# Performance work log

Hardware: AMD Instinct MI355X
Metric: run time of the kernel (lower is better)

## Reference

```python
import jax, jax.numpy as jnp
import numpy as np

T_MAX = 20  # max_seq_length


def setup_inputs() -> dict:
    key = jax.random.key(0)
    ks = jax.random.split(key, 24)
    B, H, A, V, Tc = 64, 512, 512, 50257, 19
    s = 0.02
    inp = {}
    inp["features"] = jax.random.normal(ks[0], (B, H), jnp.float32)
    inp["captions"] = jax.random.randint(ks[1], (B, Tc), 0, V)
    lens = jax.random.randint(ks[2], (B, 1), 1, T_MAX + 1)
    inp["lengths"] = -jnp.sort(-lens, axis=0)  # descending so sort_ind is identity
    inp["embed_table"] = jax.random.uniform(ks[3], (V, H), jnp.float32, -0.1, 0.1)
    # LSTM cell (PyTorch layout): input = [emb; attended] -> 2H
    inp["W_ih"] = jax.random.normal(ks[4], (4 * H, 2 * H), jnp.float32) * s
    inp["W_hh"] = jax.random.normal(ks[5], (4 * H, H), jnp.float32) * s
    inp["b_ih"] = jnp.zeros((4 * H,), jnp.float32)
    inp["b_hh"] = jnp.zeros((4 * H,), jnp.float32)
    # attention
    inp["W_enc"] = jax.random.normal(ks[6], (H, A), jnp.float32) * s
    inp["b_enc"] = jnp.zeros((A,), jnp.float32)
    inp["W_dec"] = jax.random.normal(ks[7], (H, A), jnp.float32) * s
    inp["b_dec"] = jnp.zeros((A,), jnp.float32)
    inp["W_full"] = jax.random.normal(ks[8], (A, 1), jnp.float32) * s
    inp["b_full"] = jnp.zeros((1,), jnp.float32)
    # init_h / init_c / f_beta / fc
    inp["W_hinit"] = jax.random.normal(ks[9], (H, H), jnp.float32) * s
    inp["b_hinit"] = jnp.zeros((H,), jnp.float32)
    inp["W_cinit"] = jax.random.normal(ks[10], (H, H), jnp.float32) * s
    inp["b_cinit"] = jnp.zeros((H,), jnp.float32)
    inp["W_beta"] = jax.random.normal(ks[11], (H, H), jnp.float32) * s
    inp["b_beta"] = jnp.zeros((H,), jnp.float32)
    inp["W_fc"] = jax.random.uniform(ks[12], (H, V), jnp.float32, -0.1, 0.1)
    inp["b_fc"] = jnp.zeros((V,), jnp.float32)
    return inp


def _decode(features, embed_table, W_ih, W_hh, b_ih, b_hh, W_enc, b_enc,
            W_dec, b_dec, W_full, b_full, W_hinit, b_hinit, W_cinit, b_cinit,
            W_beta, b_beta, W_fc, b_fc, captions, lengths):
    B, H = features.shape
    emb = embed_table[captions]                               # (B, T-1, H)
    embeddings = jnp.concatenate([features[:, None, :], emb], axis=1)  # (B, T, H)
    encoder_out = features[:, None, :]                        # (B, 1, H) num_pixels=1
    mean_enc = encoder_out.mean(axis=1)
    h0 = mean_enc @ W_hinit + b_hinit
    c0 = mean_enc @ W_cinit + b_cinit
    att1 = encoder_out @ W_enc + b_enc                        # (B, 1, A), time-invariant
    lens = lengths[:, 0]

    def step(carry, xs):
        h, c = carry
        emb_t, t = xs
        # attention
        att2 = h @ W_dec + b_dec                              # (B, A)
        e = jax.nn.relu(att1 + att2[:, None, :]) @ W_full + b_full  # (B, 1, 1)
        alpha = jax.nn.softmax(e[..., 0], axis=1)             # (B, 1)
        awe = (encoder_out * alpha[..., None]).sum(axis=1)    # (B, H)
        gate = jax.nn.sigmoid(h @ W_beta + b_beta)
        awe = gate * awe
        # LSTM cell (PyTorch gate order i, f, g, o)
        x = jnp.concatenate([emb_t, awe], axis=1)             # (B, 2H)
        gates = x @ W_ih.T + b_ih + h @ W_hh.T + b_hh
        i, f, g, o = jnp.split(gates, 4, axis=1)
        c_new = jax.nn.sigmoid(f) * c + jax.nn.sigmoid(i) * jnp.tanh(g)
        h_new = jax.nn.sigmoid(o) * jnp.tanh(c_new)
        preds = h_new @ W_fc + b_fc                           # (B, V)
        mask = (t < lens)[:, None]
        h = jnp.where(mask, h_new, h)
        c = jnp.where(mask, c_new, c)
        out_t = jnp.where(mask, preds, jnp.zeros_like(preds))
        return (h, c), out_t

    xs = (embeddings.transpose(1, 0, 2), jnp.arange(T_MAX))
    _, outs = jax.lax.scan(step, (h0, c0), xs)                # (T, B, V)
    return outs.transpose(1, 0, 2)                            # (B, T, V)


def reference(features, captions, lengths, embed_table, W_ih, W_hh, b_ih, b_hh,
              W_enc, b_enc, W_dec, b_dec, W_full, b_full, W_hinit, b_hinit,
              W_cinit, b_cinit, W_beta, b_beta, W_fc, b_fc):
    return _decode(features, embed_table, W_ih, W_hh, b_ih, b_hh, W_enc, b_enc,
                   W_dec, b_dec, W_full, b_full, W_hinit, b_hinit, W_cinit,
                   b_cinit, W_beta, b_beta, W_fc, b_fc, captions, lengths)
```

## Files before the change

### kernel.cpp

```cpp
#include <hip/hip_runtime.h>
#include <hip/hip_bf16.h>


#define VV 50257
#define VP 50304
#define TT 20
#define NWRK 32
#define NTILES 6288

typedef __attribute__((ext_vector_type(4))) float f32x4;
typedef __attribute__((ext_vector_type(8))) short bf16x8;

#define MFMA(a,b,c) __builtin_amdgcn_mfma_f32_16x16x32_bf16((a),(b),(c),0,0,0)

__device__ __forceinline__ unsigned short f2bf(float f){
  union { float f; unsigned int u; } v; v.f = f;
  unsigned int u = v.u;
  return (unsigned short)((u + 0x7FFFu + ((u >> 16) & 1u)) >> 16);
}
__device__ __forceinline__ float sigf(float x){ return 1.f/(1.f + expf(-x)); }

__device__ __forceinline__ void gload_lds16(const unsigned short* g, unsigned short* l){
  __builtin_amdgcn_global_load_lds(
      (const __attribute__((address_space(1))) unsigned int*)g,
      (__attribute__((address_space(3))) unsigned int*)l, 16, 0, 0);
}

__device__ __forceinline__ void l2_load16(bf16x8* d, const unsigned short* p){
  asm volatile("global_load_dwordx4 %0, %1, off sc0" : "=v"(*d) : "v"(p));
}
__device__ __forceinline__ void l2_store2(unsigned short* p, unsigned short v){
  asm volatile("global_store_short %0, %1, off sc0" :: "v"(p), "v"(v) : "memory");
}

__device__ __forceinline__ void gbar(unsigned int* flags, int widx, unsigned target){
  asm volatile("s_waitcnt vmcnt(0)" ::: "memory");
  __syncthreads();
  if(threadIdx.x == 0){
    asm volatile("global_store_dword %0, %1, off sc0 sc1"
                 :: "v"(flags + widx), "v"(target) : "memory");
  }
  if(threadIdx.x < 64){
    const unsigned int* p = flags + (threadIdx.x & 31);
    for(;;){
      unsigned v;
      asm volatile("global_load_dword %0, %1, off sc0 sc1\n\ts_waitcnt vmcnt(0)"
                   : "=v"(v) : "v"(p) : "memory");
      if(__all((int)(v >= target))) break;
      __builtin_amdgcn_s_sleep(1);
    }
  }
  __syncthreads();
}

__global__ __launch_bounds__(256) void prep(const float* __restrict__ Wih,
    const float* __restrict__ Whh, unsigned short* __restrict__ Wcomb,
    unsigned short* __restrict__ We,
    const float* __restrict__ Wbeta, unsigned short* __restrict__ Wbt,
    const float* __restrict__ feat, const float* __restrict__ emb,
    const int* __restrict__ cap, unsigned short* __restrict__ EmbMat,
    const float* __restrict__ Whi, const float* __restrict__ bhi,
    const float* __restrict__ Wci, const float* __restrict__ bci,
    unsigned short* __restrict__ xbuf, float* __restrict__ cbuf){
  __shared__ float tile[64][65];
  const int blk = blockIdx.x, tid = threadIdx.x;
  if(blk < 2048){
    int j = blk;
    for(int q=0;q<4;q++){ int k = tid + 256*q;
      float v = (k < 512) ? Whh[j*512 + k] : Wih[j*1024 + k];
      Wcomb[(size_t)j*1024 + k] = f2bf(v); }
    for(int q=0;q<2;q++){ int k = tid + 256*q;
      We[(size_t)j*512 + k] = f2bf(Wih[j*1024 + k]); }
  } else if(blk < 2112){
    int tb = blk - 2048;
    int c0 = (tb & 7)*64, r0 = (tb >> 3)*64;
    int tx = tid & 63, ty = tid >> 6;
    for(int i=0;i<16;i++){
      int r = ty + i*4;
      tile[r][tx] = Wbeta[(size_t)(r0+r)*512 + c0 + tx];
    }
    __syncthreads();
    for(int i=0;i<16;i++){
      int cl = ty + i*4;
      Wbt[(size_t)(c0+cl)*512 + r0 + tx] = f2bf(tile[tx][cl]);
    }
  } else if(blk < 3392){
    int m = blk - 2112; int t = m >> 6, b = m & 63;
    const float* src = (t == 0) ? (feat + b*512) : (emb + (size_t)cap[b*19 + (t-1)]*512);
    for(int q=0;q<2;q++){ int k = tid + 256*q;
      EmbMat[(size_t)m*512 + k] = f2bf(src[k]); }
  } else {
    int b = blk - 3392;
    float ah0 = bhi[tid], ah1 = bhi[tid+256];
    float ac0 = bci[tid], ac1 = bci[tid+256];
    for(int k=0;k<512;k++){
      float f = feat[b*512 + k];
      ah0 += f * Whi[k*512 + tid];     ah1 += f * Whi[k*512 + tid + 256];
      ac0 += f * Wci[k*512 + tid];     ac1 += f * Wci[k*512 + tid + 256];
    }
    xbuf[b*512 + tid] = f2bf(ah0);  xbuf[b*512 + tid + 256] = f2bf(ah1);
    cbuf[b*512 + tid] = ac0;        cbuf[b*512 + tid + 256] = ac1;
  }
}

template<int EPIL>
__global__ __launch_bounds__(256) void gemm2(const unsigned short* __restrict__ Abf,
    const unsigned short* __restrict__ Bbf, const float* __restrict__ bias1,
    const float* __restrict__ bias2, const int* __restrict__ lensp,
    float* __restrict__ Cout, int MT){
  __shared__ __align__(16) char smem[32768];
  unsigned short* As = (unsigned short*)smem;
  unsigned short* Bs = (unsigned short*)(smem + 16384);
  float* et = (float*)smem;

  const int nwg = gridDim.x;
  const int id = blockIdx.x;
  const int q = nwg >> 3, rr = nwg & 7;
  const int xcd = id & 7, pos = id >> 3;
  const int work = (xcd < rr) ? (xcd*(q+1) + pos) : (rr*(q+1) + (xcd-rr)*q + pos);
  const int m0 = (work % MT) * 128;
  const int n0 = (work / MT) * 128;
  const int tid = threadIdx.x, lane = tid & 63, w = tid >> 6;
  const int wr = w >> 1, wc = w & 1;
  const int lrow = lane >> 3, lcol = (lane & 7) * 8;
  const int l15 = lane & 15, lhi = lane >> 4;

  f32x4 acc[4][4];
#pragma unroll
  for(int i=0;i<4;i++)
#pragma unroll
    for(int j=0;j<4;j++) acc[i][j] = f32x4{0.f,0.f,0.f,0.f};

  for(int k0=0;k0<512;k0+=64){
    __syncthreads();
#pragma unroll
    for(int i=0;i<4;i++){
      int c = w*4 + i;
      int row = c*8 + lrow;
      gload_lds16(Abf + (size_t)(m0+row)*512 + k0 + lcol, As + c*512);
      gload_lds16(Bbf + (size_t)(n0+row)*512 + k0 + lcol, Bs + c*512);
    }
    asm volatile("s_waitcnt vmcnt(0)" ::: "memory");
    __syncthreads();
#pragma unroll
    for(int kk=0;kk<64;kk+=32){
      bf16x8 af[4], bfv[4];
#pragma unroll
      for(int mf=0;mf<4;mf++)
        af[mf] = *(const bf16x8*)(As + (wr*64 + mf*16 + l15)*64 + kk + lhi*8);
#pragma unroll
      for(int nf=0;nf<4;nf++)
        bfv[nf] = *(const bf16x8*)(Bs + (wc*64 + nf*16 + l15)*64 + kk + lhi*8);
#pragma unroll
      for(int mf=0;mf<4;mf++)
#pragma unroll
        for(int nf=0;nf<4;nf++)
          acc[mf][nf] = MFMA(af[mf], bfv[nf], acc[mf][nf]);
    }
  }

  if constexpr (EPIL == 0){
#pragma unroll
    for(int mf=0;mf<4;mf++)
#pragma unroll
      for(int nf=0;nf<4;nf++){
        int n = n0 + wc*64 + nf*16 + l15;
#pragma unroll
        for(int r=0;r<4;r++){
          int m = m0 + wr*64 + mf*16 + lhi*4 + r;
          int gate = n >> 9, col = n & 511;
          Cout[((size_t)m*512 + col)*4 + gate] = acc[mf][nf][r] + bias1[n] + bias2[n];
        }
      }
  } else {
    const bool edge = (n0 + 128 > VV);
    for(int half=0; half<2; half++){
      __syncthreads();
      if(wr == half){
#pragma unroll
        for(int mf=0;mf<4;mf++)
#pragma unroll
          for(int nf=0;nf<4;nf++){
            int n = n0 + wc*64 + nf*16 + l15;
#pragma unroll
            for(int r=0;r<4;r++){
              int m = m0 + half*64 + mf*16 + lhi*4 + r;
              int b = m/20, tt = m%20;
              float v = (tt < lensp[b]) ? (acc[mf][nf][r] + bias1[n]) : 0.f;
              et[(mf*16 + lhi*4 + r)*128 + wc*64 + nf*16 + l15] = v;
            }
          }
      }
      __syncthreads();
#pragma unroll
      for(int qq=0;qq<8;qq++){
        int idx = tid + 256*qq;
        int row = idx >> 5, c4 = idx & 31;
        int m = m0 + half*64 + row;
        const float* er = et + row*128;
        if(!edge){
          size_t bdw = (size_t)m*VV + n0;
          int al = (int)((4 - (bdw & 3)) & 3);
          int chunks = (128 - al) >> 2;
          int tail = (128 - al) & 3;
          if(c4 < chunks){
            int s0 = al + c4*4;
            f32x4 v; v[0]=er[s0]; v[1]=er[s0+1]; v[2]=er[s0+2]; v[3]=er[s0+3];
            *(f32x4*)(Cout + bdw + s0) = v;
          }
          if(c4 < al) Cout[bdw + c4] = er[c4];
          if(c4 < tail){ int s1 = al + chunks*4 + c4; Cout[bdw + s1] = er[s1]; }
        } else {
#pragma unroll
          for(int i=0;i<4;i++){
            int cg = n0 + c4*4 + i;
            if(cg < VV) Cout[(size_t)m*VV + cg] = er[c4*4 + i];
          }
        }
      }
    }
  }
}

__global__ __launch_bounds__(256) void recur(
    const unsigned short* __restrict__ Wcomb,
    const unsigned short* __restrict__ Wbt,
    const float* __restrict__ bbeta,
    const float* __restrict__ feat,
    const float* __restrict__ E4,
    const float* __restrict__ c0,
    const int* __restrict__ lens,
    unsigned short* xbuf,
    unsigned short* awbuf,
    unsigned short* __restrict__ hs,
    unsigned int* ctrs,
    const float* __restrict__ Wfc, unsigned short* __restrict__ Wfct){
  extern __shared__ char LDS[];
  char* WCb = LDS;
  char* WBb = LDS + 131072;
  int* lsh = (int*)LDS;
  const int tid = threadIdx.x;

  if(tid == 0){
    unsigned xcc = 99;
    asm volatile("s_getreg_b32 %0, hwreg(HW_REG_XCC_ID)" : "=s"(xcc));
    unsigned my = 0xffffffffu;
    if(xcc == 0) my = atomicAdd(&ctrs[0], 1u);
    lsh[0] = (my < NWRK) ? 1 : 0;
    lsh[1] = (int)my;
  }
  __syncthreads();
  const int iswork = lsh[0];
  const int widx = lsh[1];
  __syncthreads();

  if(!iswork){
    float (*tile)[65] = (float(*)[65])LDS;
    int tx = tid & 63, ty = tid >> 6;
    for(;;){
      __syncthreads();
      if(tid == 0) lsh[0] = (int)atomicAdd(&ctrs[16], 1u);
      __syncthreads();
      int tb = lsh[0];
      __syncthreads();
      if(tb >= NTILES) return;
      int c0t = (tb % 786)*64, r0 = (tb / 786)*64;
      for(int i=0;i<16;i++){
        int r = ty + i*4; int sc = c0t + tx;
        tile[r][tx] = (sc < VV) ? Wfc[(size_t)(r0+r)*VV + sc] : 0.f;
      }
      __syncthreads();
      for(int i=0;i<16;i++){
        int cl = ty + i*4;
        Wfct[(size_t)(c0t+cl)*512 + r0 + tx] = f2bf(tile[tx][cl]);
      }
    }
  }

  const int lane = tid & 63, w = tid >> 6;
  const int l15 = lane & 15, lhi = lane >> 4;
  const int jj0 = widx * 16;
  const int jj = jj0 + l15;
  const int arow = w*16 + l15;
  unsigned int* flags = &ctrs[32];

  for(int cid = tid; cid < 8192; cid += 256){
    int gr = cid >> 7, cc = cid & 127;
    size_t g = (size_t)(gr >> 4)*512 + jj0 + (gr & 15);
    bf16x8 v = *(const bf16x8*)(Wcomb + g*1024 + cc*8);
    *(bf16x8*)(WCb + gr*2048 + ((cc*16) ^ ((gr & 7) << 4))) = v;
  }
  for(int cid = tid; cid < 1024; cid += 256){
    int r = cid >> 6, cc = cid & 63;
    bf16x8 v = *(const bf16x8*)(Wbt + (size_t)(jj0 + r)*512 + cc*8);
    *(bf16x8*)(WBb + r*1024 + ((cc*16) ^ ((r & 7) << 4))) = v;
  }

  float c_reg[4], fe[4]; int ln[4]; unsigned short hold[4];
#pragma unroll
  for(int r=0;r<4;r++){
    int b = w*16 + lhi*4 + r;
    c_reg[r] = c0[b*512 + jj];
    fe[r]    = feat[b*512 + jj];
    ln[r]    = lens[b];
    hold[r]  = xbuf[b*512 + jj];
  }
  const float bb = bbeta[jj];
  const unsigned short* pAx = xbuf  + (size_t)arow*512 + lhi*8;
  const unsigned short* pAw = awbuf + (size_t)arow*512 + lhi*8;
  __syncthreads();

  for(int t=0;t<TT;t++){
    bf16x8 a[16];
#pragma unroll
    for(int i=0;i<16;i++) l2_load16(&a[i], pAx + i*32);
    asm volatile("s_waitcnt vmcnt(0)" ::: "memory");
    __builtin_amdgcn_sched_barrier(0);

    f32x4 acca = f32x4{0.f,0.f,0.f,0.f};
    f32x4 accg[4];
#pragma unroll
    for(int i=0;i<4;i++) accg[i] = f32x4{0.f,0.f,0.f,0.f};
#pragma unroll
    for(int i=0;i<16;i++){
      int kb2 = i*64 + lhi*16;
      bf16x8 wb = *(const bf16x8*)(WBb + l15*1024 + (kb2 ^ ((l15 & 7) << 4)));
      acca = MFMA(a[i], wb, acca);
#pragma unroll
      for(int nf=0; nf<4; nf++){
        int gr = nf*16 + l15;
        bf16x8 wg = *(const bf16x8*)(WCb + gr*2048 + (kb2 ^ ((gr & 7) << 4)));
        accg[nf] = MFMA(a[i], wg, accg[nf]);
      }
    }
#pragma unroll
    for(int r=0;r<4;r++){
      int b = w*16 + lhi*4 + r;
      float g = sigf(acca[r] + bb);
      l2_store2(awbuf + b*512 + jj, f2bf(g * fe[r]));
    }
    gbar(flags, widx, (unsigned)(2*t+1));

    f32x4 e4v[4];
#pragma unroll
    for(int r=0;r<4;r++){
      int b = w*16 + lhi*4 + r;
      e4v[r] = *(const f32x4*)(E4 + (((size_t)(t*64 + b))*512 + jj)*4);
    }
#pragma unroll
    for(int i=0;i<16;i++) l2_load16(&a[i], pAw + i*32);
    asm volatile("s_waitcnt vmcnt(0)" ::: "memory");
    __builtin_amdgcn_sched_barrier(0);
#pragma unroll
    for(int i=0;i<16;i++){
      int kb2 = 1024 + i*64 + lhi*16;
#pragma unroll
      for(int nf=0; nf<4; nf++){
        int gr = nf*16 + l15;
        bf16x8 wg = *(const bf16x8*)(WCb + gr*2048 + (kb2 ^ ((gr & 7) << 4)));
        accg[nf] = MFMA(a[i], wg, accg[nf]);
      }
    }

#pragma unroll
    for(int r=0;r<4;r++){
      int b = w*16 + lhi*4 + r;
      float iv = sigf(accg[0][r] + e4v[r][0]);
      float fv = sigf(accg[1][r] + e4v[r][1]);
      float gv = tanhf(accg[2][r] + e4v[r][2]);
      float ov = sigf(accg[3][r] + e4v[r][3]);
      float cn = fv*c_reg[r] + iv*gv;
      float hn = ov * tanhf(cn);
      bool valid = t < ln[r];
      if(valid) c_reg[r] = cn;
      unsigned short hb = valid ? f2bf(hn) : hold[r];
      hold[r] = hb;
      hs[((size_t)(b*20 + t))*512 + jj] = hb;
      l2_store2(xbuf + b*512 + jj, hb);
    }
    if(t < TT-1) gbar(flags, widx, (unsigned)(2*t+2));
  }
}

extern "C" void kernel_launch(void* const* d_in, const int* in_sizes, int n_in,
                              void* d_out, int out_size, void* d_ws, size_t ws_size,
                              hipStream_t stream){
  const float* feat  = (const float*)d_in[0];
  const int*   cap   = (const int*)  d_in[1];
  const int*   lens  = (const int*)  d_in[2];
  const float* emb   = (const float*)d_in[3];
  const float* Wih   = (const float*)d_in[4];
  const float* Whh   = (const float*)d_in[5];
  const float* bih   = (const float*)d_in[6];
  const float* bhh   = (const float*)d_in[7];
  const float* Whi   = (const float*)d_in[14];
  const float* bhi   = (const float*)d_in[15];
  const float* Wci   = (const float*)d_in[16];
  const float* bci   = (const float*)d_in[17];
  const float* Wbeta = (const float*)d_in[18];
  const float* bbeta = (const float*)d_in[19];
  const float* Wfc   = (const float*)d_in[20];
  const float* bfc   = (const float*)d_in[21];
  float* out = (float*)d_out;

  char* ws = (char*)d_ws;
  size_t off = 0;
  auto alloc = [&](size_t bytes)->void*{
    void* p = ws + off; off += (bytes + 1023) & ~(size_t)1023; return p; };
  unsigned short* Wcomb  = (unsigned short*)alloc((size_t)2048*1024*2);
  unsigned short* We     = (unsigned short*)alloc((size_t)2048*512*2);
  unsigned short* Wbt    = (unsigned short*)alloc((size_t)512*512*2);
  unsigned short* Wfct   = (unsigned short*)alloc((size_t)VP*512*2);
  unsigned short* EmbMat = (unsigned short*)alloc((size_t)1280*512*2);
  float*          E4     = (float*)alloc((size_t)1280*2048*4);
  unsigned short* xbuf   = (unsigned short*)alloc((size_t)64*512*2);
  unsigned short* awbuf  = (unsigned short*)alloc((size_t)64*512*2);
  float*          cbuf   = (float*)alloc((size_t)64*512*4);
  unsigned short* hs     = (unsigned short*)alloc((size_t)1280*512*2);
  unsigned int*   ctrs   = (unsigned int*)alloc(256);

  static_cast<void>(hipFuncSetAttribute((const void*)recur,
      hipFuncAttributeMaxDynamicSharedMemorySize, 147456));

  hipMemsetAsync(ctrs, 0, 256, stream);

  prep<<<3456, 256, 0, stream>>>(Wih, Whh, Wcomb, We, Wbeta, Wbt, feat, emb,
                                 cap, EmbMat, Whi, bhi, Wci, bci, xbuf, cbuf);

  gemm2<0><<<160, 256, 0, stream>>>(EmbMat, We, bih, bhh, nullptr, E4, 10);

  recur<<<2080, 256, 147456, stream>>>(Wcomb, Wbt, bbeta, feat, E4, cbuf, lens,
                                       xbuf, awbuf, hs, ctrs, Wfc, Wfct);

  gemm2<1><<<3930, 256, 0, stream>>>(hs, Wfct, bfc, nullptr, lens, out, 10);
}
```

Before: 598.3 us.

## Fuse vocab projection into persistent recurrence kernel, overlapping per-timestep GEMM

The final vocabulary GEMM becomes work items inside the persistent recurrent kernel. Idle (non-recurrent) workgroups first transpose W_fc, then pull per-timestep output tiles from an atomic queue. Each tile waits on the barrier flags for its timestep before computing from the h states, which are now stored time-major with LLC-coherent stores. This lets the large output GEMM overlap with the serial LSTM steps and drops a separate launch, at the cost of spin-waiting, a persistent grid of 256 blocks, and a 64-row M tile that is less efficient per job.

New measurement: 660.5 us. 10.4% more time.

```diff
diff --git a/kernel.cpp b/kernel.cpp
--- a/kernel.cpp
+++ b/kernel.cpp
@@ -7,6 +7,8 @@
 #define TT 20
 #define NWRK 32
 #define NTILES 6288
+#define NNT 393
+#define NGJOBS (TT*NNT)
 
 typedef __attribute__((ext_vector_type(4))) float f32x4;
 typedef __attribute__((ext_vector_type(8))) short bf16x8;
@@ -31,6 +33,15 @@
 }
 __device__ __forceinline__ void l2_store2(unsigned short* p, unsigned short v){
   asm volatile("global_store_short %0, %1, off sc0" :: "v"(p), "v"(v) : "memory");
+}
+__device__ __forceinline__ void llc_store2(unsigned short* p, unsigned short v){
+  asm volatile("global_store_short %0, %1, off sc0 sc1" :: "v"(p), "v"(v) : "memory");
+}
+__device__ __forceinline__ unsigned int llc_load_u32(const unsigned int* p){
+  unsigned int r;
+  asm volatile("global_load_dword %0, %1, off sc0 sc1\n\ts_waitcnt vmcnt(0)"
+               : "=v"(r) : "v"(p) : "memory");
+  return r;
 }
 
 __device__ __forceinline__ void gbar(unsigned int* flags, int widx, unsigned target){
@@ -43,9 +54,7 @@
   if(threadIdx.x < 64){
     const unsigned int* p = flags + (threadIdx.x & 31);
     for(;;){
-      unsigned v;
-      asm volatile("global_load_dword %0, %1, off sc0 sc1\n\ts_waitcnt vmcnt(0)"
-                   : "=v"(v) : "v"(p) : "memory");
+      unsigned v = llc_load_u32(p);
       if(__all((int)(v >= target))) break;
       __builtin_amdgcn_s_sleep(1);
     }
@@ -103,16 +112,11 @@
   }
 }
 
-template<int EPIL>
-__global__ __launch_bounds__(256) void gemm2(const unsigned short* __restrict__ Abf,
+__global__ __launch_bounds__(256) void gemmE(const unsigned short* __restrict__ Abf,
     const unsigned short* __restrict__ Bbf, const float* __restrict__ bias1,
-    const float* __restrict__ bias2, const int* __restrict__ lensp,
-    float* __restrict__ Cout, int MT){
-  __shared__ __align__(16) char smem[32768];
-  unsigned short* As = (unsigned short*)smem;
-  unsigned short* Bs = (unsigned short*)(smem + 16384);
-  float* et = (float*)smem;
-
+    const float* __restrict__ bias2, float* __restrict__ Cout, int MT){
+  __shared__ __align__(16) unsigned short As[128*64];
+  __shared__ __align__(16) unsigned short Bs[128*64];
   const int nwg = gridDim.x;
   const int id = blockIdx.x;
   const int q = nwg >> 3, rr = nwg & 7;
@@ -158,68 +162,18 @@
           acc[mf][nf] = MFMA(af[mf], bfv[nf], acc[mf][nf]);
     }
   }
-
-  if constexpr (EPIL == 0){
-#pragma unroll
-    for(int mf=0;mf<4;mf++)
-#pragma unroll
-      for(int nf=0;nf<4;nf++){
-        int n = n0 + wc*64 + nf*16 + l15;
-#pragma unroll
-        for(int r=0;r<4;r++){
-          int m = m0 + wr*64 + mf*16 + lhi*4 + r;
-          int gate = n >> 9, col = n & 511;
-          Cout[((size_t)m*512 + col)*4 + gate] = acc[mf][nf][r] + bias1[n] + bias2[n];
-        }
-      }
-  } else {
-    const bool edge = (n0 + 128 > VV);
-    for(int half=0; half<2; half++){
-      __syncthreads();
-      if(wr == half){
-#pragma unroll
-        for(int mf=0;mf<4;mf++)
-#pragma unroll
-          for(int nf=0;nf<4;nf++){
-            int n = n0 + wc*64 + nf*16 + l15;
-#pragma unroll
-            for(int r=0;r<4;r++){
-              int m = m0 + half*64 + mf*16 + lhi*4 + r;
-              int b = m/20, tt = m%20;
-              float v = (tt < lensp[b]) ? (acc[mf][nf][r] + bias1[n]) : 0.f;
-              et[(mf*16 + lhi*4 + r)*128 + wc*64 + nf*16 + l15] = v;
-            }
-          }
-      }
-      __syncthreads();
-#pragma unroll
-      for(int qq=0;qq<8;qq++){
-        int idx = tid + 256*qq;
-        int row = idx >> 5, c4 = idx & 31;
-        int m = m0 + half*64 + row;
-        const float* er = et + row*128;
-        if(!edge){
-          size_t bdw = (size_t)m*VV + n0;
-          int al = (int)((4 - (bdw & 3)) & 3);
-          int chunks = (128 - al) >> 2;
-          int tail = (128 - al) & 3;
-          if(c4 < chunks){
-            int s0 = al + c4*4;
-            f32x4 v; v[0]=er[s0]; v[1]=er[s0+1]; v[2]=er[s0+2]; v[3]=er[s0+3];
-            *(f32x4*)(Cout + bdw + s0) = v;
-          }
-          if(c4 < al) Cout[bdw + c4] = er[c4];
-          if(c4 < tail){ int s1 = al + chunks*4 + c4; Cout[bdw + s1] = er[s1]; }
-        } else {
-#pragma unroll
-          for(int i=0;i<4;i++){
-            int cg = n0 + c4*4 + i;
-            if(cg < VV) Cout[(size_t)m*VV + cg] = er[c4*4 + i];
-          }
-        }
-      }
-    }
-  }
+#pragma unroll
+  for(int mf=0;mf<4;mf++)
+#pragma unroll
+    for(int nf=0;nf<4;nf++){
+      int n = n0 + wc*64 + nf*16 + l15;
+#pragma unroll
+      for(int r=0;r<4;r++){
+        int m = m0 + wr*64 + mf*16 + lhi*4 + r;
+        int gate = n >> 9, col = n & 511;
+        Cout[((size_t)m*512 + col)*4 + gate] = acc[mf][nf][r] + bias1[n] + bias2[n];
+      }
+    }
 }
 
 __global__ __launch_bounds__(256) void recur(
@@ -232,12 +186,11 @@
     const int* __restrict__ lens,
     unsigned short* xbuf,
     unsigned short* awbuf,
-    unsigned short* __restrict__ hs,
+    unsigned short* hs,
     unsigned int* ctrs,
-    const float* __restrict__ Wfc, unsigned short* __restrict__ Wfct){
+    const float* __restrict__ Wfc, unsigned short* Wfct,
+    const float* __restrict__ bfc, float* __restrict__ out){
   extern __shared__ char LDS[];
-  char* WCb = LDS;
-  char* WBb = LDS + 131072;
   int* lsh = (int*)LDS;
   const int tid = threadIdx.x;
 
@@ -252,42 +205,165 @@
   __syncthreads();
   const int iswork = lsh[0];
   const int widx = lsh[1];
+  unsigned int* flags = &ctrs[32];
   __syncthreads();
 
   if(!iswork){
+    const int lane = tid & 63, w = tid >> 6;
+    const int lrow = lane >> 3, lcol = (lane & 7)*8;
+    const int l15 = lane & 15, lhi = lane >> 4;
+    unsigned short* As = (unsigned short*)LDS;
+    unsigned short* Bs = (unsigned short*)(LDS + 8192);
+    float* et = (float*)LDS;
     float (*tile)[65] = (float(*)[65])LDS;
-    int tx = tid & 63, ty = tid >> 6;
+    int* tk = (int*)(LDS + 147440);
+    bool tdone = false;
+
     for(;;){
       __syncthreads();
-      if(tid == 0) lsh[0] = (int)atomicAdd(&ctrs[16], 1u);
+      if(tid == 0) *tk = (int)atomicAdd(&ctrs[1], 1u);
       __syncthreads();
-      int tb = lsh[0];
+      int j = *tk;
       __syncthreads();
-      if(tb >= NTILES) return;
-      int c0t = (tb % 786)*64, r0 = (tb / 786)*64;
-      for(int i=0;i<16;i++){
-        int r = ty + i*4; int sc = c0t + tx;
-        tile[r][tx] = (sc < VV) ? Wfc[(size_t)(r0+r)*VV + sc] : 0.f;
+      if(j >= NTILES + NGJOBS) return;
+
+      if(j < NTILES){
+        int c0t = (j % 786)*64, r0 = (j / 786)*64;
+        int tx = tid & 63, ty = tid >> 6;
+        for(int i=0;i<16;i++){
+          int r = ty + i*4; int sc = c0t + tx;
+          tile[r][tx] = (sc < VV) ? Wfc[(size_t)(r0+r)*VV + sc] : 0.f;
+        }
+        __syncthreads();
+        for(int i=0;i<16;i++){
+          int cl = ty + i*4;
+          llc_store2(Wfct + (size_t)(c0t+cl)*512 + r0 + tx, f2bf(tile[tx][cl]));
+        }
+        asm volatile("s_waitcnt vmcnt(0)" ::: "memory");
+        __syncthreads();
+        if(tid == 0) atomicAdd(&ctrs[2], 1u);
+        continue;
+      }
+
+      int g = j - NTILES;
+      int t = g / NNT, nt = g % NNT;
+      int n0 = nt * 128;
+      if(!tdone){
+        if(tid == 0){
+          while(llc_load_u32(&ctrs[2]) < NTILES) __builtin_amdgcn_s_sleep(8);
+        }
+        __syncthreads();
+        tdone = true;
+      }
+      if(tid < 64){
+        const unsigned int* p = flags + (tid & 31);
+        unsigned tgt = (unsigned)(2*t + 2);
+        for(;;){
+          unsigned v = llc_load_u32(p);
+          if(__all((int)(v >= tgt))) break;
+          __builtin_amdgcn_s_sleep(4);
+        }
       }
       __syncthreads();
-      for(int i=0;i<16;i++){
-        int cl = ty + i*4;
-        Wfct[(size_t)(c0t+cl)*512 + r0 + tx] = f2bf(tile[tx][cl]);
-      }
-    }
-  }
-
+
+      f32x4 acc[4][2];
+#pragma unroll
+      for(int i=0;i<4;i++){ acc[i][0] = f32x4{0.f,0.f,0.f,0.f};
+                            acc[i][1] = f32x4{0.f,0.f,0.f,0.f}; }
+      for(int k0=0;k0<512;k0+=64){
+        __syncthreads();
+        if(w < 2){
+#pragma unroll
+          for(int i=0;i<4;i++){
+            int c = w*4 + i; int row = c*8 + lrow;
+            gload_lds16(hs + (size_t)(t*64 + row)*512 + k0 + lcol, As + c*512);
+          }
+        }
+#pragma unroll
+        for(int i=0;i<4;i++){
+          int c = w*4 + i; int row = c*8 + lrow;
+          gload_lds16(Wfct + (size_t)(n0 + row)*512 + k0 + lcol, Bs + c*512);
+        }
+        asm volatile("s_waitcnt vmcnt(0)" ::: "memory");
+        __syncthreads();
+#pragma unroll
+        for(int kk=0;kk<64;kk+=32){
+          bf16x8 af[4], bv[2];
+#pragma unroll
+          for(int mf=0;mf<4;mf++)
+            af[mf] = *(const bf16x8*)(As + (mf*16 + l15)*64 + kk + lhi*8);
+#pragma unroll
+          for(int nf=0;nf<2;nf++)
+            bv[nf] = *(const bf16x8*)(Bs + (w*32 + nf*16 + l15)*64 + kk + lhi*8);
+#pragma unroll
+          for(int mf=0;mf<4;mf++){
+            acc[mf][0] = MFMA(af[mf], bv[0], acc[mf][0]);
+            acc[mf][1] = MFMA(af[mf], bv[1], acc[mf][1]);
+          }
+        }
+      }
+      __syncthreads();
+      float bias[2];
+#pragma unroll
+      for(int nf=0;nf<2;nf++){
+        int n = n0 + w*32 + nf*16 + l15;
+        bias[nf] = (n < VV) ? bfc[n] : 0.f;
+      }
+#pragma unroll
+      for(int mf=0;mf<4;mf++){
+#pragma unroll
+        for(int r=0;r<4;r++){
+          int row = mf*16 + lhi*4 + r;
+          bool valid = t < lens[row];
+#pragma unroll
+          for(int nf=0;nf<2;nf++){
+            float v = valid ? (acc[mf][nf][r] + bias[nf]) : 0.f;
+            et[row*128 + w*32 + nf*16 + l15] = v;
+          }
+        }
+      }
+      __syncthreads();
+      const bool edge = (n0 + 128 > VV);
+#pragma unroll
+      for(int qq=0;qq<8;qq++){
+        int idx = tid + 256*qq;
+        int row = idx >> 5, c4 = idx & 31;
+        const float* er = et + row*128;
+        size_t bdw = (size_t)(row*20 + t)*VV + n0;
+        if(!edge){
+          int al = (int)((4 - (bdw & 3)) & 3);
+          int chunks = (128 - al) >> 2;
+          int tail = (128 - al) & 3;
+          if(c4 < chunks){
+            int s0 = al + c4*4;
+            f32x4 v; v[0]=er[s0]; v[1]=er[s0+1]; v[2]=er[s0+2]; v[3]=er[s0+3];
+            *(f32x4*)(out + bdw + s0) = v;
+          }
+          if(c4 < al) out[bdw + c4] = er[c4];
+          if(c4 < tail){ int s1 = al + chunks*4 + c4; out[bdw + s1] = er[s1]; }
+        } else {
+#pragma unroll
+          for(int i=0;i<4;i++){
+            int cg = n0 + c4*4 + i;
+            if(cg < VV) out[bdw + (c4*4 + i)] = er[c4*4 + i];
+          }
+        }
+      }
+    }
+  }
+
+  char* WCb = LDS;
+  char* WBb = LDS + 131072;
   const int lane = tid & 63, w = tid >> 6;
   const int l15 = lane & 15, lhi = lane >> 4;
   const int jj0 = widx * 16;
   const int jj = jj0 + l15;
   const int arow = w*16 + l15;
-  unsigned int* flags = &ctrs[32];
 
   for(int cid = tid; cid < 8192; cid += 256){
     int gr = cid >> 7, cc = cid & 127;
-    size_t g = (size_t)(gr >> 4)*512 + jj0 + (gr & 15);
-    bf16x8 v = *(const bf16x8*)(Wcomb + g*1024 + cc*8);
+    size_t gg = (size_t)(gr >> 4)*512 + jj0 + (gr & 15);
+    bf16x8 v = *(const bf16x8*)(Wcomb + gg*1024 + cc*8);
     *(bf16x8*)(WCb + gr*2048 + ((cc*16) ^ ((gr & 7) << 4))) = v;
   }
   for(int cid = tid; cid < 1024; cid += 256){
@@ -375,10 +451,10 @@
       if(valid) c_reg[r] = cn;
       unsigned short hb = valid ? f2bf(hn) : hold[r];
       hold[r] = hb;
-      hs[((size_t)(b*20 + t))*512 + jj] = hb;
+      llc_store2(hs + (size_t)(t*64 + b)*512 + jj, hb);
       l2_store2(xbuf + b*512 + jj, hb);
     }
-    if(t < TT-1) gbar(flags, widx, (unsigned)(2*t+2));
+    gbar(flags, widx, (unsigned)(2*t+2));
   }
 }
 
@@ -427,10 +503,8 @@
   prep<<<3456, 256, 0, stream>>>(Wih, Whh, Wcomb, We, Wbeta, Wbt, feat, emb,
                                  cap, EmbMat, Whi, bhi, Wci, bci, xbuf, cbuf);
 
-  gemm2<0><<<160, 256, 0, stream>>>(EmbMat, We, bih, bhh, nullptr, E4, 10);
-
-  recur<<<2080, 256, 147456, stream>>>(Wcomb, Wbt, bbeta, feat, E4, cbuf, lens,
-                                       xbuf, awbuf, hs, ctrs, Wfc, Wfct);
-
-  gemm2<1><<<3930, 256, 0, stream>>>(hs, Wfct, bfc, nullptr, lens, out, 10);
-}
+  gemmE<<<160, 256, 0, stream>>>(EmbMat, We, bih, bhh, E4, 10);
+
+  recur<<<256, 256, 147456, stream>>>(Wcomb, Wbt, bbeta, feat, E4, cbuf, lens,
+                                      xbuf, awbuf, hs, ctrs, Wfc, Wfct, bfc, out);
+}
```
